# Kernel optimization log

Hardware: AMD Instinct MI355X
Metric: run time of the kernel (lower is better)

Reference implementation:

```python
import jax, jax.numpy as jnp
import numpy as np

N = 100000   # nodes (in_ch)
D = 128      # emb_ch
E = 1600000  # nonzeros in A_hat
RATE = 0.1   # dropout rate


def setup_inputs() -> dict:
    key = jax.random.key(0)
    k1, k2, k3, k4, k5, k6 = jax.random.split(key, 6)
    x = jnp.arange(N, dtype=jnp.int64) if jax.config.jax_enable_x64 else jnp.arange(N, dtype=jnp.int32)
    rows = jax.random.randint(k1, (E,), 0, N)
    cols = jax.random.randint(k2, (E,), 0, N)
    A_vals = jax.random.uniform(k3, (E,), dtype=jnp.float32)
    # xavier_uniform for [N, D]: bound = sqrt(6/(N+D))
    bound = float(np.sqrt(6.0 / (N + D)))
    emb_weight = jax.random.uniform(k4, (N, D), jnp.float32, -bound, bound)
    u1 = jax.random.uniform(k5, (N, D), dtype=jnp.float32)
    u2 = jax.random.uniform(k6, (N, D), dtype=jnp.float32)
    return {"x": x, "rows": rows, "cols": cols, "A_vals": A_vals,
            "emb_weight": emb_weight, "u1": u1, "u2": u2}


def _dropout(h, u):
    keep = (u >= RATE).astype(h.dtype)
    return h * keep / (1.0 - RATE)


def _spmm(rows, cols, vals, h):
    # out[i] = sum_{e: rows[e]==i} vals[e] * h[cols[e]]  -- COO SpMM
    msgs = vals[:, None] * h[cols]  # [E, D]
    return jax.ops.segment_sum(msgs, rows, num_segments=N)


def reference(x, rows, cols, A_vals, emb_weight, u1, u2):
    h0 = emb_weight[x]                       # embedding lookup [N, D]
    h1 = _spmm(rows, cols, A_vals, _dropout(h0, u1))
    h2 = _spmm(rows, cols, A_vals, _dropout(h1, u2))
    return (h0 + h1 + h2) / 3.0
```

## Files before the change

### kernel.cpp

```cpp
#include <hip/hip_runtime.h>
#include <hip/hip_fp16.h>

#define DD 128
#define SCAN_CHUNK 1024
#define ROWS_PER_BLK 16
#define MAX_STAGE 512

typedef float          f32x4 __attribute__((ext_vector_type(4)));
typedef unsigned int   u32x4 __attribute__((ext_vector_type(4)));
typedef unsigned int   u32x2 __attribute__((ext_vector_type(2)));
typedef unsigned short u16x8 __attribute__((ext_vector_type(8)));

struct __align__(8) Edge { int c; float v; };

__device__ __forceinline__ unsigned short f2h(float f) {
    return __half_as_ushort(__float2half(f));
}
__device__ __forceinline__ float2 up2(unsigned int u) {
    __half2 h = *reinterpret_cast<const __half2*>(&u);
    return __half22float2(h);
}

template <typename T>
__device__ __forceinline__ T ldnt(const T* p) { return __builtin_nontemporal_load(p); }
template <typename T>
__device__ __forceinline__ void stnt(T* p, T v) { __builtin_nontemporal_store(v, p); }


__global__ __launch_bounds__(256) void k_zero(int* __restrict__ p, int n) {
    int i = blockIdx.x * 256 + threadIdx.x;
    if (i < n) p[i] = 0;
}

__global__ __launch_bounds__(256) void k_prep(const float* __restrict__ emb,
                                              const float* __restrict__ u1,
                                              const float* __restrict__ u2,
                                              ushort* __restrict__ g1,
                                              ushort* __restrict__ emb16,
                                              unsigned char* __restrict__ mask2,
                                              int total8, int prepBlocks,
                                              const int* __restrict__ rows,
                                              int* __restrict__ cnt, int E) {
    if ((int)blockIdx.x < prepBlocks) {
        int i = blockIdx.x * 256 + threadIdx.x;
        if (i >= total8) return;
        const f32x4* e4 = (const f32x4*)emb;
        const f32x4* a4 = (const f32x4*)u1;
        const f32x4* b4 = (const f32x4*)u2;
        f32x4 hA = ldnt(e4 + 2 * (size_t)i);
        f32x4 hB = ldnt(e4 + 2 * (size_t)i + 1);
        f32x4 uA = ldnt(a4 + 2 * (size_t)i);
        f32x4 uB = ldnt(a4 + 2 * (size_t)i + 1);
        f32x4 vA = ldnt(b4 + 2 * (size_t)i);
        f32x4 vB = ldnt(b4 + 2 * (size_t)i + 1);
        const float s = 1.0f / 0.9f;
        u16x8 g;
        g[0] = f2h((uA.x >= 0.1f) ? hA.x * s : 0.0f);
        g[1] = f2h((uA.y >= 0.1f) ? hA.y * s : 0.0f);
        g[2] = f2h((uA.z >= 0.1f) ? hA.z * s : 0.0f);
        g[3] = f2h((uA.w >= 0.1f) ? hA.w * s : 0.0f);
        g[4] = f2h((uB.x >= 0.1f) ? hB.x * s : 0.0f);
        g[5] = f2h((uB.y >= 0.1f) ? hB.y * s : 0.0f);
        g[6] = f2h((uB.z >= 0.1f) ? hB.z * s : 0.0f);
        g[7] = f2h((uB.w >= 0.1f) ? hB.w * s : 0.0f);
        ((u16x8*)g1)[i] = g;
        u16x8 e16;
        e16[0] = f2h(hA.x); e16[1] = f2h(hA.y); e16[2] = f2h(hA.z); e16[3] = f2h(hA.w);
        e16[4] = f2h(hB.x); e16[5] = f2h(hB.y); e16[6] = f2h(hB.z); e16[7] = f2h(hB.w);
        stnt((u16x8*)emb16 + i, e16);
        unsigned char m =
            (unsigned char)((vA.x >= 0.1f ? 1u : 0u)  | (vA.y >= 0.1f ? 2u : 0u)  |
                            (vA.z >= 0.1f ? 4u : 0u)  | (vA.w >= 0.1f ? 8u : 0u)  |
                            (vB.x >= 0.1f ? 16u : 0u) | (vB.y >= 0.1f ? 32u : 0u) |
                            (vB.z >= 0.1f ? 64u : 0u) | (vB.w >= 0.1f ? 128u : 0u));
        stnt(mask2 + i, m);
    } else {
        int e = ((int)blockIdx.x - prepBlocks) * 256 + threadIdx.x;
        if (e < E) {
            int r = ldnt(rows + e);
            atomicAdd(&cnt[r], 1);
        }
    }
}

__global__ __launch_bounds__(256) void k_scan1(int* __restrict__ data,
                                               int* __restrict__ bsum, int n) {
    __shared__ int s[256];
    int tid = threadIdx.x;
    int base = blockIdx.x * SCAN_CHUNK + tid * 4;
    int v0 = 0, v1 = 0, v2 = 0, v3 = 0;
    if (base + 0 < n) v0 = data[base + 0];
    if (base + 1 < n) v1 = data[base + 1];
    if (base + 2 < n) v2 = data[base + 2];
    if (base + 3 < n) v3 = data[base + 3];
    int tsum = v0 + v1 + v2 + v3;
    s[tid] = tsum;
    __syncthreads();
    for (int off = 1; off < 256; off <<= 1) {
        int t = (tid >= off) ? s[tid - off] : 0;
        __syncthreads();
        s[tid] += t;
        __syncthreads();
    }
    int excl = s[tid] - tsum;
    if (tid == 255) bsum[blockIdx.x] = s[255];
    if (base + 0 < n) data[base + 0] = excl;
    if (base + 1 < n) data[base + 1] = excl + v0;
    if (base + 2 < n) data[base + 2] = excl + v0 + v1;
    if (base + 3 < n) data[base + 3] = excl + v0 + v1 + v2;
}

__global__ __launch_bounds__(256) void k_scan23(int* __restrict__ data,
                                                const int* __restrict__ bsum,
                                                int* __restrict__ cursor,
                                                int nb, int n) {
    __shared__ int s[1024];
    int tid = threadIdx.x;
    for (int i = tid; i < nb; i += 256) s[i] = bsum[i];
    __syncthreads();
    if (tid == 0) {
        int run = 0;
        for (int i = 0; i < nb; ++i) { int t = s[i]; s[i] = run; run += t; }
    }
    __syncthreads();
    int i = blockIdx.x * 256 + tid;
    if (i < n) {
        int v = data[i] + s[i >> 10];
        data[i] = v;
        cursor[i] = v;
    }
}

__global__ __launch_bounds__(256) void k_scatter(const int* __restrict__ rows,
                                                 const int* __restrict__ cols,
                                                 const float* __restrict__ vals,
                                                 int* __restrict__ cursor,
                                                 Edge* __restrict__ ev, int E) {
    int e = blockIdx.x * 256 + threadIdx.x;
    if (e >= E) return;
    int r = ldnt(rows + e);
    int c = ldnt(cols + e);
    float v = ldnt(vals + e);
    int pos = atomicAdd(&cursor[r], 1);
    u32x2 q;
    q.x = (unsigned int)c;
    q.y = __float_as_uint(v);
    ((u32x2*)ev)[pos] = q;
}

template <int MODE>
__global__ __launch_bounds__(256) void k_gather(const int* __restrict__ rowstart,
                                                const Edge* __restrict__ ev,
                                                const ushort* __restrict__ srch,
                                                const unsigned char* __restrict__ mask2,
                                                const ushort* __restrict__ emb16,
                                                const ushort* __restrict__ p16in,
                                                ushort* __restrict__ p16out,
                                                ushort* __restrict__ g2,
                                                float* __restrict__ out,
                                                int N, int E) {
    __shared__ int s_rs[ROWS_PER_BLK + 1];
    __shared__ Edge s_ev[MAX_STAGE];

    int tid = threadIdx.x;
    int r0 = blockIdx.x * ROWS_PER_BLK;
    if (tid <= ROWS_PER_BLK) {
        int r = r0 + tid;
        s_rs[tid] = (r < N) ? rowstart[r] : E;
    }
    __syncthreads();
    int base = s_rs[0];
    int nblk = s_rs[ROWS_PER_BLK] - base;
    int nstage = nblk < MAX_STAGE ? nblk : MAX_STAGE;
    for (int i = tid; i < nstage; i += 256) {
        u32x2 q = ldnt((const u32x2*)(ev + base + i));
        Edge ed; ed.c = (int)q.x; ed.v = __uint_as_float(q.y);
        s_ev[i] = ed;
    }
    __syncthreads();

    int grp = tid >> 4;
    int lane = tid & 15;
    int row = r0 + grp;
    if (row >= N) return;
    int start = s_rs[grp] - base;
    int end = s_rs[grp + 1] - base;
    int eL = end < nstage ? end : nstage;

    const u32x4* __restrict__ s4 = (const u32x4*)srch;
    const Edge* __restrict__ evg = ev + base;
    float a0 = 0.f, a1 = 0.f, a2 = 0.f, a3 = 0.f;
    float a4 = 0.f, a5 = 0.f, a6 = 0.f, a7 = 0.f;

#define LDE(i) Edge E##i = s_ev[e + i];
#define GQ(i)  u32x4 q##i = s4[((size_t)E##i.c << 4) + lane];
#define ACC(i) { float vv = E##i.v; \
        float2 w0 = up2(q##i.x), w1 = up2(q##i.y), w2 = up2(q##i.z), w3 = up2(q##i.w); \
        a0 = fmaf(vv, w0.x, a0); a1 = fmaf(vv, w0.y, a1); \
        a2 = fmaf(vv, w1.x, a2); a3 = fmaf(vv, w1.y, a3); \
        a4 = fmaf(vv, w2.x, a4); a5 = fmaf(vv, w2.y, a5); \
        a6 = fmaf(vv, w3.x, a6); a7 = fmaf(vv, w3.y, a7); }

    int e = start;
    for (; e + 8 <= eL; e += 8) {
        LDE(0) LDE(1) LDE(2) LDE(3) LDE(4) LDE(5) LDE(6) LDE(7)
        GQ(0) GQ(1) GQ(2) GQ(3) GQ(4) GQ(5) GQ(6) GQ(7)
        ACC(0) ACC(1) ACC(2) ACC(3) ACC(4) ACC(5) ACC(6) ACC(7)
    }
    if (e + 4 <= eL) {
        LDE(0) LDE(1) LDE(2) LDE(3)
        GQ(0) GQ(1) GQ(2) GQ(3)
        ACC(0) ACC(1) ACC(2) ACC(3)
        e += 4;
    }
    for (; e < eL; ++e) {
        LDE(0) GQ(0) ACC(0)
    }
    for (; e < end; ++e) {
        Edge E0; { u32x2 q_ = ldnt((const u32x2*)(evg + e));
                   E0.c = (int)q_.x; E0.v = __uint_as_float(q_.y); }
        GQ(0) ACC(0)
    }
#undef LDE
#undef GQ
#undef ACC

    size_t o = ((size_t)row << 7) + (size_t)lane * 8;
    if (MODE == 1) {
        unsigned int m = ldnt(mask2 + (size_t)row * 16 + lane);
        const float s = 1.0f / 0.9f;
        u16x8 gg;
        gg[0] = (m & 1u)   ? f2h(a0 * s) : (ushort)0;
        gg[1] = (m & 2u)   ? f2h(a1 * s) : (ushort)0;
        gg[2] = (m & 4u)   ? f2h(a2 * s) : (ushort)0;
        gg[3] = (m & 8u)   ? f2h(a3 * s) : (ushort)0;
        gg[4] = (m & 16u)  ? f2h(a4 * s) : (ushort)0;
        gg[5] = (m & 32u)  ? f2h(a5 * s) : (ushort)0;
        gg[6] = (m & 64u)  ? f2h(a6 * s) : (ushort)0;
        gg[7] = (m & 128u) ? f2h(a7 * s) : (ushort)0;
        stnt((u16x8*)(g2 + o), gg);
        u16x8 pp;
        pp[0] = f2h(a0); pp[1] = f2h(a1); pp[2] = f2h(a2); pp[3] = f2h(a3);
        pp[4] = f2h(a4); pp[5] = f2h(a5); pp[6] = f2h(a6); pp[7] = f2h(a7);
        stnt((u16x8*)(p16out + o), pp);
    } else {
        u32x4 eq = ldnt((const u32x4*)(emb16 + o));
        u32x4 pq = ldnt((const u32x4*)(p16in + o));
        float2 e0 = up2(eq.x), e1 = up2(eq.y), e2 = up2(eq.z), e3 = up2(eq.w);
        float2 p0 = up2(pq.x), p1 = up2(pq.y), p2 = up2(pq.z), p3 = up2(pq.w);
        const float t3 = 1.0f / 3.0f;
        f32x4 rA, rB;
        rA.x = (e0.x + p0.x + a0) * t3;
        rA.y = (e0.y + p0.y + a1) * t3;
        rA.z = (e1.x + p1.x + a2) * t3;
        rA.w = (e1.y + p1.y + a3) * t3;
        rB.x = (e2.x + p2.x + a4) * t3;
        rB.y = (e2.y + p2.y + a5) * t3;
        rB.z = (e3.x + p3.x + a6) * t3;
        rB.w = (e3.y + p3.y + a7) * t3;
        stnt((f32x4*)(out + o), rA);
        stnt((f32x4*)(out + o) + 1, rB);
    }
}


extern "C" void kernel_launch(void* const* d_in, const int* in_sizes, int n_in,
                              void* d_out, int out_size, void* d_ws, size_t ws_size,
                              hipStream_t stream) {
    const int* rows = (const int*)d_in[1];
    const int* cols = (const int*)d_in[2];
    const float* vals = (const float*)d_in[3];
    const float* emb = (const float*)d_in[4];
    const float* u1 = (const float*)d_in[5];
    const float* u2 = (const float*)d_in[6];
    float* out = (float*)d_out;

    const int N = in_sizes[0];
    const int E = in_sizes[1];
    const size_t ND = (size_t)N * DD;

    char* ws = (char*)d_ws;
    Edge* ev     = (Edge*)ws;   ws += (size_t)E * sizeof(Edge);
    ushort* g1   = (ushort*)ws; ws += ND * sizeof(ushort);
    ushort* g2   = (ushort*)ws; ws += ND * sizeof(ushort);
    ushort* p16  = (ushort*)ws; ws += ND * sizeof(ushort);
    ushort* emb16= (ushort*)ws; ws += ND * sizeof(ushort);
    int* cnt     = (int*)ws;    ws += (size_t)N * sizeof(int);
    int* cursor  = (int*)ws;    ws += (size_t)N * sizeof(int);
    int* bsum    = (int*)ws;    ws += 4096;
    unsigned char* mask2 = (unsigned char*)ws;

    const int total8 = (int)(ND / 8);
    const int prepBlocks = (total8 + 255) / 256;
    const int gridE = (E + 255) / 256;
    const int gridN = (N + 255) / 256;
    const int nScanBlocks = (N + SCAN_CHUNK - 1) / SCAN_CHUNK;
    const int gridRow = (N + ROWS_PER_BLK - 1) / ROWS_PER_BLK;

    k_zero<<<gridN, 256, 0, stream>>>(cnt, N);
    k_prep<<<prepBlocks + gridE, 256, 0, stream>>>(emb, u1, u2, g1, emb16, mask2,
                                                   total8, prepBlocks, rows, cnt, E);
    k_scan1<<<nScanBlocks, 256, 0, stream>>>(cnt, bsum, N);
    k_scan23<<<gridN, 256, 0, stream>>>(cnt, bsum, cursor, nScanBlocks, N);
    k_scatter<<<gridE, 256, 0, stream>>>(rows, cols, vals, cursor, ev, E);

    k_gather<1><<<gridRow, 256, 0, stream>>>(cnt, ev, g1, mask2, nullptr, nullptr,
                                             p16, g2, nullptr, N, E);
    k_gather<2><<<gridRow, 256, 0, stream>>>(cnt, ev, g2, nullptr, emb16, p16,
                                             nullptr, nullptr, out, N, E);
}
```

Baseline: 455.7 us.

## Record atomic ranks in histogram pass to drop scatter atomics and rebalance prep

The histogram pass now stores each edge's atomicAdd return value as its rank within the row. The scatter pass can then compute its position as rowstart plus rank with no second atomic. The dense prep work is split across two kernels: g1 is built alongside the histogram, and emb16 and mask2 are built alongside the scatter, so each fused kernel overlaps streaming loads with edge work. The zero kernel is replaced by hipMemsetAsync and the cursor array is removed, at the cost of an extra E-sized rank buffer written and read back.

```diff
diff --git a/kernel.cpp b/kernel.cpp
--- a/kernel.cpp
+++ b/kernel.cpp
@@ -26,33 +26,26 @@
 template <typename T>
 __device__ __forceinline__ void stnt(T* p, T v) { __builtin_nontemporal_store(v, p); }
 
-
-__global__ __launch_bounds__(256) void k_zero(int* __restrict__ p, int n) {
+__global__ __launch_bounds__(256) void k_g1hist(const float* __restrict__ emb,
+                                                const float* __restrict__ u1,
+                                                ushort* __restrict__ g1,
+                                                const int* __restrict__ rows,
+                                                int* __restrict__ cnt,
+                                                int* __restrict__ rank,
+                                                int total8, int E) {
     int i = blockIdx.x * 256 + threadIdx.x;
-    if (i < n) p[i] = 0;
-}
-
-__global__ __launch_bounds__(256) void k_prep(const float* __restrict__ emb,
-                                              const float* __restrict__ u1,
-                                              const float* __restrict__ u2,
-                                              ushort* __restrict__ g1,
-                                              ushort* __restrict__ emb16,
-                                              unsigned char* __restrict__ mask2,
-                                              int total8, int prepBlocks,
-                                              const int* __restrict__ rows,
-                                              int* __restrict__ cnt, int E) {
-    if ((int)blockIdx.x < prepBlocks) {
-        int i = blockIdx.x * 256 + threadIdx.x;
-        if (i >= total8) return;
+    if (i < E) {
+        int r = ldnt(rows + i);
+        int old = atomicAdd(&cnt[r], 1);
+        stnt(rank + i, old);
+    }
+    if (i < total8) {
         const f32x4* e4 = (const f32x4*)emb;
         const f32x4* a4 = (const f32x4*)u1;
-        const f32x4* b4 = (const f32x4*)u2;
         f32x4 hA = ldnt(e4 + 2 * (size_t)i);
         f32x4 hB = ldnt(e4 + 2 * (size_t)i + 1);
         f32x4 uA = ldnt(a4 + 2 * (size_t)i);
         f32x4 uB = ldnt(a4 + 2 * (size_t)i + 1);
-        f32x4 vA = ldnt(b4 + 2 * (size_t)i);
-        f32x4 vB = ldnt(b4 + 2 * (size_t)i + 1);
         const float s = 1.0f / 0.9f;
         u16x8 g;
         g[0] = f2h((uA.x >= 0.1f) ? hA.x * s : 0.0f);
@@ -64,22 +57,6 @@
         g[6] = f2h((uB.z >= 0.1f) ? hB.z * s : 0.0f);
         g[7] = f2h((uB.w >= 0.1f) ? hB.w * s : 0.0f);
         ((u16x8*)g1)[i] = g;
-        u16x8 e16;
-        e16[0] = f2h(hA.x); e16[1] = f2h(hA.y); e16[2] = f2h(hA.z); e16[3] = f2h(hA.w);
-        e16[4] = f2h(hB.x); e16[5] = f2h(hB.y); e16[6] = f2h(hB.z); e16[7] = f2h(hB.w);
-        stnt((u16x8*)emb16 + i, e16);
-        unsigned char m =
-            (unsigned char)((vA.x >= 0.1f ? 1u : 0u)  | (vA.y >= 0.1f ? 2u : 0u)  |
-                            (vA.z >= 0.1f ? 4u : 0u)  | (vA.w >= 0.1f ? 8u : 0u)  |
-                            (vB.x >= 0.1f ? 16u : 0u) | (vB.y >= 0.1f ? 32u : 0u) |
-                            (vB.z >= 0.1f ? 64u : 0u) | (vB.w >= 0.1f ? 128u : 0u));
-        stnt(mask2 + i, m);
-    } else {
-        int e = ((int)blockIdx.x - prepBlocks) * 256 + threadIdx.x;
-        if (e < E) {
-            int r = ldnt(rows + e);
-            atomicAdd(&cnt[r], 1);
-        }
     }
 }
 
@@ -112,7 +89,6 @@
 
 __global__ __launch_bounds__(256) void k_scan23(int* __restrict__ data,
                                                 const int* __restrict__ bsum,
-                                                int* __restrict__ cursor,
                                                 int nb, int n) {
     __shared__ int s[1024];
     int tid = threadIdx.x;
@@ -124,28 +100,50 @@
     }
     __syncthreads();
     int i = blockIdx.x * 256 + tid;
-    if (i < n) {
-        int v = data[i] + s[i >> 10];
-        data[i] = v;
-        cursor[i] = v;
-    }
-}
-
-__global__ __launch_bounds__(256) void k_scatter(const int* __restrict__ rows,
-                                                 const int* __restrict__ cols,
-                                                 const float* __restrict__ vals,
-                                                 int* __restrict__ cursor,
-                                                 Edge* __restrict__ ev, int E) {
-    int e = blockIdx.x * 256 + threadIdx.x;
-    if (e >= E) return;
-    int r = ldnt(rows + e);
-    int c = ldnt(cols + e);
-    float v = ldnt(vals + e);
-    int pos = atomicAdd(&cursor[r], 1);
-    u32x2 q;
-    q.x = (unsigned int)c;
-    q.y = __float_as_uint(v);
-    ((u32x2*)ev)[pos] = q;
+    if (i < n) data[i] += s[i >> 10];
+}
+
+__global__ __launch_bounds__(256) void k_scatter_prep(const int* __restrict__ rows,
+                                                      const int* __restrict__ cols,
+                                                      const float* __restrict__ vals,
+                                                      const int* __restrict__ rowstart,
+                                                      const int* __restrict__ rank,
+                                                      Edge* __restrict__ ev,
+                                                      const float* __restrict__ emb,
+                                                      const float* __restrict__ u2,
+                                                      ushort* __restrict__ emb16,
+                                                      unsigned char* __restrict__ mask2,
+                                                      int E, int total8) {
+    int i = blockIdx.x * 256 + threadIdx.x;
+    if (i < E) {
+        int r = ldnt(rows + i);
+        int c = ldnt(cols + i);
+        float v = ldnt(vals + i);
+        int rk = ldnt(rank + i);
+        int pos = rowstart[r] + rk;
+        u32x2 q;
+        q.x = (unsigned int)c;
+        q.y = __float_as_uint(v);
+        ((u32x2*)ev)[pos] = q;
+    }
+    if (i < total8) {
+        const f32x4* e4 = (const f32x4*)emb;
+        const f32x4* b4 = (const f32x4*)u2;
+        f32x4 hA = ldnt(e4 + 2 * (size_t)i);
+        f32x4 hB = ldnt(e4 + 2 * (size_t)i + 1);
+        f32x4 vA = ldnt(b4 + 2 * (size_t)i);
+        f32x4 vB = ldnt(b4 + 2 * (size_t)i + 1);
+        u16x8 e16;
+        e16[0] = f2h(hA.x); e16[1] = f2h(hA.y); e16[2] = f2h(hA.z); e16[3] = f2h(hA.w);
+        e16[4] = f2h(hB.x); e16[5] = f2h(hB.y); e16[6] = f2h(hB.z); e16[7] = f2h(hB.w);
+        stnt((u16x8*)emb16 + i, e16);
+        unsigned char m =
+            (unsigned char)((vA.x >= 0.1f ? 1u : 0u)  | (vA.y >= 0.1f ? 2u : 0u)  |
+                            (vA.z >= 0.1f ? 4u : 0u)  | (vA.w >= 0.1f ? 8u : 0u)  |
+                            (vB.x >= 0.1f ? 16u : 0u) | (vB.y >= 0.1f ? 32u : 0u) |
+                            (vB.z >= 0.1f ? 64u : 0u) | (vB.w >= 0.1f ? 128u : 0u));
+        stnt(mask2 + i, m);
+    }
 }
 
 template <int MODE>
@@ -286,24 +284,23 @@
     ushort* p16  = (ushort*)ws; ws += ND * sizeof(ushort);
     ushort* emb16= (ushort*)ws; ws += ND * sizeof(ushort);
     int* cnt     = (int*)ws;    ws += (size_t)N * sizeof(int);
-    int* cursor  = (int*)ws;    ws += (size_t)N * sizeof(int);
+    int* rank    = (int*)ws;    ws += (size_t)E * sizeof(int);
     int* bsum    = (int*)ws;    ws += 4096;
     unsigned char* mask2 = (unsigned char*)ws;
 
     const int total8 = (int)(ND / 8);
     const int prepBlocks = (total8 + 255) / 256;
     const int gridE = (E + 255) / 256;
-    const int gridN = (N + 255) / 256;
+    const int gridFuse = prepBlocks > gridE ? prepBlocks : gridE;
     const int nScanBlocks = (N + SCAN_CHUNK - 1) / SCAN_CHUNK;
     const int gridRow = (N + ROWS_PER_BLK - 1) / ROWS_PER_BLK;
 
-    k_zero<<<gridN, 256, 0, stream>>>(cnt, N);
-    k_prep<<<prepBlocks + gridE, 256, 0, stream>>>(emb, u1, u2, g1, emb16, mask2,
-                                                   total8, prepBlocks, rows, cnt, E);
+    hipMemsetAsync(cnt, 0, (size_t)N * sizeof(int), stream);
+    k_g1hist<<<gridFuse, 256, 0, stream>>>(emb, u1, g1, rows, cnt, rank, total8, E);
     k_scan1<<<nScanBlocks, 256, 0, stream>>>(cnt, bsum, N);
-    k_scan23<<<gridN, 256, 0, stream>>>(cnt, bsum, cursor, nScanBlocks, N);
-    k_scatter<<<gridE, 256, 0, stream>>>(rows, cols, vals, cursor, ev, E);
-
+    k_scan23<<<(N + 255) / 256, 256, 0, stream>>>(cnt, bsum, nScanBlocks, N);
+    k_scatter_prep<<<gridFuse, 256, 0, stream>>>(rows, cols, vals, cnt, rank, ev,
+                                                 emb, u2, emb16, mask2, E, total8);
     k_gather<1><<<gridRow, 256, 0, stream>>>(cnt, ev, g1, mask2, nullptr, nullptr,
                                              p16, g2, nullptr, N, E);
     k_gather<2><<<gridRow, 256, 0, stream>>>(cnt, ev, g2, nullptr, emb16, p16,
```

Result: faster. 411.3 us (-9.7%).
